# Performance work log

Measured on AMD Instinct MI355X. Metric: run time of the kernel, lower is better.

Reference implementation:

```python
import jax, jax.numpy as jnp
from jax import lax
import numpy as np

I, H, O = 4, 64, 4  # input_size, hidden_size, fc out


def setup_inputs() -> dict:
    key = jax.random.key(0)
    ks = jax.random.split(key, 7)
    B, T = 2048, 512
    s_ih = 1.0 / np.sqrt(H)  # PyTorch default init scale
    x = jax.random.normal(ks[0], (B, T, I), dtype=jnp.float32)
    W_ih = jax.random.uniform(ks[1], (4 * H, I), minval=-s_ih, maxval=s_ih, dtype=jnp.float32)
    W_hh = jax.random.uniform(ks[2], (4 * H, H), minval=-s_ih, maxval=s_ih, dtype=jnp.float32)
    b_ih = jax.random.uniform(ks[3], (4 * H,), minval=-s_ih, maxval=s_ih, dtype=jnp.float32)
    b_hh = jax.random.uniform(ks[4], (4 * H,), minval=-s_ih, maxval=s_ih, dtype=jnp.float32)
    W_fc = jax.random.uniform(ks[5], (O, H), minval=-s_ih, maxval=s_ih, dtype=jnp.float32)
    b_fc = jax.random.uniform(ks[6], (O,), minval=-s_ih, maxval=s_ih, dtype=jnp.float32)
    return {"x": x, "W_ih": W_ih, "W_hh": W_hh, "b_ih": b_ih, "b_hh": b_hh,
            "W_fc": W_fc, "b_fc": b_fc}


def reference(x, W_ih, W_hh, b_ih, b_hh, W_fc, b_fc):
    B = x.shape[0]
    # Precompute input contribution to all gates for every timestep: [B, T, 4H]
    xg = jnp.einsum('bti,gi->btg', x, W_ih) + (b_ih + b_hh)

    def step(carry, xt):
        h, c = carry                      # [B, H], [B, H]
        gates = xt + h @ W_hh.T           # [B, 4H]; PyTorch gate order i,f,g,o
        i, f, g, o = jnp.split(gates, 4, axis=-1)
        c = jax.nn.sigmoid(f) * c + jax.nn.sigmoid(i) * jnp.tanh(g)
        h = jax.nn.sigmoid(o) * jnp.tanh(c)
        return (h, c), None

    h0 = jnp.zeros((B, H), dtype=x.dtype)
    (h, c), _ = lax.scan(step, (h0, h0), jnp.swapaxes(xg, 0, 1))  # scan over T
    hidden = h[None]                      # [1, B, H] (num_layers*dirs = 1)
    return hidden @ W_fc.T + b_fc         # [1, B, O]
```

## Files before the change

kernel.cpp:

```cpp
#include <hip/hip_runtime.h>

typedef _Float16 half8 __attribute__((ext_vector_type(8)));
typedef _Float16 half4 __attribute__((ext_vector_type(4)));
typedef float f32x4 __attribute__((ext_vector_type(4)));

#define TT 512
#define HH 64
#define MB 4
#define S  88
#define XS 2056

__global__ __launch_bounds__(256, 2)
void lstm_v13(const float* __restrict__ x,
              const float* __restrict__ W_ih,
              const float* __restrict__ W_hh,
              const float* __restrict__ b_ih,
              const float* __restrict__ b_hh,
              const float* __restrict__ W_fc,
              const float* __restrict__ b_fc,
              float* __restrict__ out)
{
    __shared__ __align__(16) _Float16 st[2][MB * S];
    __shared__ __align__(16) _Float16 xbuf[MB * XS];

    const int tid = threadIdx.x;
    const int w   = tid >> 6;
    const int l   = tid & 63;
    const int q   = l >> 4;
    const int col = l & 15;
    const int bt  = col & 3;
    const int g   = col >> 2;
    const int b0  = blockIdx.x * MB;

    const float kN = -1.4426950408889634f;
    const float kP =  2.8853900817779268f;

    half8 aw[4][3];
    #pragma unroll
    for (int p = 0; p < 4; ++p) {
        const int r = 64 * (col & 3) + 16 * w + 4 * p + (col >> 2);
        const float scale = ((col & 3) == 2) ? kP : kN;
        #pragma unroll
        for (int c = 0; c < 2; ++c) {
            const float* src = W_hh + r * HH + 32 * c + 8 * q;
            half8 v;
            #pragma unroll
            for (int j = 0; j < 8; ++j) v[j] = (_Float16)(src[j] * scale);
            aw[p][c] = v;
        }
        half8 v = {};
        if (q == 0) {
            #pragma unroll
            for (int j = 0; j < 4; ++j) v[j] = (_Float16)(W_ih[r * 4 + j] * scale);
            v[4] = (_Float16)((b_ih[r] + b_hh[r]) * scale);
        }
        aw[p][2] = v;
    }

    #pragma unroll
    for (int it = 0; it < (MB * TT) / 256; ++it) {
        const int task = tid + it * 256;
        const int b = task >> 9, t = task & 511;
        float4 v = *(const float4*)(x + ((size_t)(b0 + b) * TT + t) * 4);
        half4 hx;
        hx[0] = (_Float16)v.x; hx[1] = (_Float16)v.y;
        hx[2] = (_Float16)v.z; hx[3] = (_Float16)v.w;
        *(half4*)&xbuf[b * XS + t * 4] = hx;
    }

    for (int i = tid; i < 2 * MB * S; i += 256) (&st[0][0])[i] = (_Float16)0.f;
    __syncthreads();

    float cs = 0.f;
    const int wrow = bt * S + 16 * w + 4 * g + q;
    const _Float16 hone = (_Float16)1.0f, hzer = (_Float16)0.f;
    const f32x4 z4 = {0.f, 0.f, 0.f, 0.f};
    const bool s1 = (g & 1) != 0, s2 = (g & 2) != 0;

    f32x4 accx0, accx1, accx2, accx3;
    {
        half4 xv = *(const half4*)&xbuf[bt * XS + 0];
        half8 bx = {xv[0], xv[1], xv[2], xv[3], hone, hzer, hzer, hzer};
        accx0 = __builtin_amdgcn_mfma_f32_16x16x32_f16(aw[0][2], bx, z4, 0, 0, 0);
        accx1 = __builtin_amdgcn_mfma_f32_16x16x32_f16(aw[1][2], bx, z4, 0, 0, 0);
        accx2 = __builtin_amdgcn_mfma_f32_16x16x32_f16(aw[2][2], bx, z4, 0, 0, 0);
        accx3 = __builtin_amdgcn_mfma_f32_16x16x32_f16(aw[3][2], bx, z4, 0, 0, 0);
    }

    #pragma unroll 4
    for (int t = 0; t < TT; ++t) {
        const int rb = t & 1, wb = rb ^ 1;
        const _Float16* sr = &st[rb][0];

        half8 bh0 = *(const half8*)&sr[bt * S +      8 * q];
        half8 bh1 = *(const half8*)&sr[bt * S + 32 + 8 * q];
        half4 xv2 = *(const half4*)&xbuf[bt * XS + (t + 1) * 4];

        f32x4 a0 = __builtin_amdgcn_mfma_f32_16x16x32_f16(aw[0][0], bh0, accx0, 0, 0, 0);
        f32x4 a1 = __builtin_amdgcn_mfma_f32_16x16x32_f16(aw[1][0], bh0, accx1, 0, 0, 0);
        f32x4 a2 = __builtin_amdgcn_mfma_f32_16x16x32_f16(aw[2][0], bh0, accx2, 0, 0, 0);
        f32x4 a3 = __builtin_amdgcn_mfma_f32_16x16x32_f16(aw[3][0], bh0, accx3, 0, 0, 0);
        a0 = __builtin_amdgcn_mfma_f32_16x16x32_f16(aw[0][1], bh1, a0, 0, 0, 0);
        a1 = __builtin_amdgcn_mfma_f32_16x16x32_f16(aw[1][1], bh1, a1, 0, 0, 0);
        a2 = __builtin_amdgcn_mfma_f32_16x16x32_f16(aw[2][1], bh1, a2, 0, 0, 0);
        a3 = __builtin_amdgcn_mfma_f32_16x16x32_f16(aw[3][1], bh1, a3, 0, 0, 0);

        {
            half8 bx2 = {xv2[0], xv2[1], xv2[2], xv2[3], hone, hzer, hzer, hzer};
            accx0 = __builtin_amdgcn_mfma_f32_16x16x32_f16(aw[0][2], bx2, z4, 0, 0, 0);
            accx1 = __builtin_amdgcn_mfma_f32_16x16x32_f16(aw[1][2], bx2, z4, 0, 0, 0);
            accx2 = __builtin_amdgcn_mfma_f32_16x16x32_f16(aw[2][2], bx2, z4, 0, 0, 0);
            accx3 = __builtin_amdgcn_mfma_f32_16x16x32_f16(aw[3][2], bx2, z4, 0, 0, 0);
        }

        #define SEL(j) (s2 ? (s1 ? a3[j] : a2[j]) : (s1 ? a1[j] : a0[j]))
        const float gi = SEL(0);
        const float gf = SEL(1);
        const float gg = SEL(2);
        const float go = SEL(3);
        #undef SEL

        const float EI = __builtin_amdgcn_exp2f(gi);
        const float EF = __builtin_amdgcn_exp2f(gf);
        const float EG = __builtin_amdgcn_exp2f(gg);
        const float rF = __builtin_amdgcn_rcpf(1.f + EF);
        const float r1 = __builtin_amdgcn_rcpf((1.f + EI) * (EG + 1.f));
        cs = cs * rF + (EG - 1.f) * r1;
        const float EO = __builtin_amdgcn_exp2f(go);
        const float EC = __builtin_amdgcn_exp2f(kP * cs);
        const float r2 = __builtin_amdgcn_rcpf((1.f + EO) * (EC + 1.f));
        const float hn = (EC - 1.f) * r2;

        st[wb][wrow] = (_Float16)hn;
        __syncthreads();
    }

    if (tid < MB * 4) {
        const int b = tid >> 2, o = tid & 3;
        float s = b_fc[o];
        const float* wf = W_fc + o * HH;
        #pragma unroll
        for (int k = 0; k < HH; ++k)
            s = fmaf((float)st[0][b * S + k], wf[k], s);
        out[(size_t)(b0 + b) * 4 + o] = s;
    }
}

extern "C" void kernel_launch(void* const* d_in, const int* in_sizes, int n_in,
                              void* d_out, int out_size, void* d_ws, size_t ws_size,
                              hipStream_t stream) {
    const float* x    = (const float*)d_in[0];
    const float* W_ih = (const float*)d_in[1];
    const float* W_hh = (const float*)d_in[2];
    const float* b_ih = (const float*)d_in[3];
    const float* b_hh = (const float*)d_in[4];
    const float* W_fc = (const float*)d_in[5];
    const float* b_fc = (const float*)d_in[6];
    float* out = (float*)d_out;
    lstm_v13<<<2048 / MB, 256, 0, stream>>>(x, W_ih, W_hh, b_ih, b_hh, W_fc, b_fc, out);
}
```

Before: 247.8 us.

## Split LSTM gate rows across 16 waves with 8 batches per block

Restructures the recurrent LSTM kernel to launch 1024-thread blocks holding 8 sequences each. Each wave now owns 4 hidden units (16 gate rows) and issues 3 MFMAs per step instead of 12. The MFMA columns carry 8 batches instead of 4 duplicated ones, which removes redundant matrix work and the per-lane gate-select logic. The cost is a block-wide barrier across 16 waves at every timestep, and half of the lanes compute duplicate columns that are never written.

```diff
diff --git a/kernel.cpp b/kernel.cpp
--- a/kernel.cpp
+++ b/kernel.cpp
@@ -6,12 +6,12 @@
 
 #define TT 512
 #define HH 64
-#define MB 4
-#define S  88
+#define MB 8
+#define S  80
 #define XS 2056
 
-__global__ __launch_bounds__(256, 2)
-void lstm_v13(const float* __restrict__ x,
+__global__ __launch_bounds__(1024, 1)
+void lstm_v14(const float* __restrict__ x,
               const float* __restrict__ W_ih,
               const float* __restrict__ W_hh,
               const float* __restrict__ b_ih,
@@ -28,17 +28,15 @@
     const int l   = tid & 63;
     const int q   = l >> 4;
     const int col = l & 15;
-    const int bt  = col & 3;
-    const int g   = col >> 2;
+    const int bt  = col & 7;
     const int b0  = blockIdx.x * MB;
 
     const float kN = -1.4426950408889634f;
     const float kP =  2.8853900817779268f;
 
-    half8 aw[4][3];
-    #pragma unroll
-    for (int p = 0; p < 4; ++p) {
-        const int r = 64 * (col & 3) + 16 * w + 4 * p + (col >> 2);
+    half8 aw[3];
+    {
+        const int r = 64 * (col & 3) + 4 * w + (col >> 2);
         const float scale = ((col & 3) == 2) ? kP : kN;
         #pragma unroll
         for (int c = 0; c < 2; ++c) {
@@ -46,7 +44,7 @@
             half8 v;
             #pragma unroll
             for (int j = 0; j < 8; ++j) v[j] = (_Float16)(src[j] * scale);
-            aw[p][c] = v;
+            aw[c] = v;
         }
         half8 v = {};
         if (q == 0) {
@@ -54,12 +52,12 @@
             for (int j = 0; j < 4; ++j) v[j] = (_Float16)(W_ih[r * 4 + j] * scale);
             v[4] = (_Float16)((b_ih[r] + b_hh[r]) * scale);
         }
-        aw[p][2] = v;
+        aw[2] = v;
     }
 
     #pragma unroll
-    for (int it = 0; it < (MB * TT) / 256; ++it) {
-        const int task = tid + it * 256;
+    for (int it = 0; it < (MB * TT) / 1024; ++it) {
+        const int task = tid + it * 1024;
         const int b = task >> 9, t = task & 511;
         float4 v = *(const float4*)(x + ((size_t)(b0 + b) * TT + t) * 4);
         half4 hx;
@@ -68,23 +66,20 @@
         *(half4*)&xbuf[b * XS + t * 4] = hx;
     }
 
-    for (int i = tid; i < 2 * MB * S; i += 256) (&st[0][0])[i] = (_Float16)0.f;
+    for (int i = tid; i < 2 * MB * S; i += 1024) (&st[0][0])[i] = (_Float16)0.f;
     __syncthreads();
 
     float cs = 0.f;
-    const int wrow = bt * S + 16 * w + 4 * g + q;
+    const int wrow = bt * S + 4 * w + q;
+    const bool writer = (col < 8);
     const _Float16 hone = (_Float16)1.0f, hzer = (_Float16)0.f;
     const f32x4 z4 = {0.f, 0.f, 0.f, 0.f};
-    const bool s1 = (g & 1) != 0, s2 = (g & 2) != 0;
 
-    f32x4 accx0, accx1, accx2, accx3;
+    f32x4 accx;
     {
         half4 xv = *(const half4*)&xbuf[bt * XS + 0];
         half8 bx = {xv[0], xv[1], xv[2], xv[3], hone, hzer, hzer, hzer};
-        accx0 = __builtin_amdgcn_mfma_f32_16x16x32_f16(aw[0][2], bx, z4, 0, 0, 0);
-        accx1 = __builtin_amdgcn_mfma_f32_16x16x32_f16(aw[1][2], bx, z4, 0, 0, 0);
-        accx2 = __builtin_amdgcn_mfma_f32_16x16x32_f16(aw[2][2], bx, z4, 0, 0, 0);
-        accx3 = __builtin_amdgcn_mfma_f32_16x16x32_f16(aw[3][2], bx, z4, 0, 0, 0);
+        accx = __builtin_amdgcn_mfma_f32_16x16x32_f16(aw[2], bx, z4, 0, 0, 0);
     }
 
     #pragma unroll 4
@@ -96,29 +91,18 @@
         half8 bh1 = *(const half8*)&sr[bt * S + 32 + 8 * q];
         half4 xv2 = *(const half4*)&xbuf[bt * XS + (t + 1) * 4];
 
-        f32x4 a0 = __builtin_amdgcn_mfma_f32_16x16x32_f16(aw[0][0], bh0, accx0, 0, 0, 0);
-        f32x4 a1 = __builtin_amdgcn_mfma_f32_16x16x32_f16(aw[1][0], bh0, accx1, 0, 0, 0);
-        f32x4 a2 = __builtin_amdgcn_mfma_f32_16x16x32_f16(aw[2][0], bh0, accx2, 0, 0, 0);
-        f32x4 a3 = __builtin_amdgcn_mfma_f32_16x16x32_f16(aw[3][0], bh0, accx3, 0, 0, 0);
-        a0 = __builtin_amdgcn_mfma_f32_16x16x32_f16(aw[0][1], bh1, a0, 0, 0, 0);
-        a1 = __builtin_amdgcn_mfma_f32_16x16x32_f16(aw[1][1], bh1, a1, 0, 0, 0);
-        a2 = __builtin_amdgcn_mfma_f32_16x16x32_f16(aw[2][1], bh1, a2, 0, 0, 0);
-        a3 = __builtin_amdgcn_mfma_f32_16x16x32_f16(aw[3][1], bh1, a3, 0, 0, 0);
+        f32x4 a0 = __builtin_amdgcn_mfma_f32_16x16x32_f16(aw[0], bh0, accx, 0, 0, 0);
+        a0 = __builtin_amdgcn_mfma_f32_16x16x32_f16(aw[1], bh1, a0, 0, 0, 0);
 
         {
             half8 bx2 = {xv2[0], xv2[1], xv2[2], xv2[3], hone, hzer, hzer, hzer};
-            accx0 = __builtin_amdgcn_mfma_f32_16x16x32_f16(aw[0][2], bx2, z4, 0, 0, 0);
-            accx1 = __builtin_amdgcn_mfma_f32_16x16x32_f16(aw[1][2], bx2, z4, 0, 0, 0);
-            accx2 = __builtin_amdgcn_mfma_f32_16x16x32_f16(aw[2][2], bx2, z4, 0, 0, 0);
-            accx3 = __builtin_amdgcn_mfma_f32_16x16x32_f16(aw[3][2], bx2, z4, 0, 0, 0);
+            accx = __builtin_amdgcn_mfma_f32_16x16x32_f16(aw[2], bx2, z4, 0, 0, 0);
         }
 
-        #define SEL(j) (s2 ? (s1 ? a3[j] : a2[j]) : (s1 ? a1[j] : a0[j]))
-        const float gi = SEL(0);
-        const float gf = SEL(1);
-        const float gg = SEL(2);
-        const float go = SEL(3);
-        #undef SEL
+        const float gi = a0[0];
+        const float gf = a0[1];
+        const float gg = a0[2];
+        const float go = a0[3];
 
         const float EI = __builtin_amdgcn_exp2f(gi);
         const float EF = __builtin_amdgcn_exp2f(gf);
@@ -131,7 +115,7 @@
         const float r2 = __builtin_amdgcn_rcpf((1.f + EO) * (EC + 1.f));
         const float hn = (EC - 1.f) * r2;
 
-        st[wb][wrow] = (_Float16)hn;
+        if (writer) st[wb][wrow] = (_Float16)hn;
         __syncthreads();
     }
 
@@ -157,5 +141,5 @@
     const float* W_fc = (const float*)d_in[5];
     const float* b_fc = (const float*)d_in[6];
     float* out = (float*)d_out;
-    lstm_v13<<<2048 / MB, 256, 0, stream>>>(x, W_ih, W_hh, b_ih, b_hh, W_fc, b_fc, out);
+    lstm_v14<<<2048 / MB, 1024, 0, stream>>>(x, W_ih, W_hh, b_ih, b_hh, W_fc, b_fc, out);
 }
```

New measurement: 247.7 us. Within noise of the previous version (-0.1%).

## Split LSTM hidden rows across eight waves with two MFMA tiles each

Applied to the files above, without the earlier changes.

The block grows from 4 to 8 wavefronts, and each wave now owns 8 hidden units, so it issues 2 gate tiles per step instead of 4. This shortens the serial per-step MFMA chain and cuts register use, which allows more blocks per CU. The x buffer is stored pre-padded as half8 with the bias one already in place, which removes per-step vector construction. In exchange, half the lanes compute redundant gate values that are never written, and the per-step barrier now synchronises twice as many waves.

```diff
diff --git a/kernel.cpp b/kernel.cpp
--- a/kernel.cpp
+++ b/kernel.cpp
@@ -7,11 +7,11 @@
 #define TT 512
 #define HH 64
 #define MB 4
-#define S  88
-#define XS 2056
+#define S  80
+#define XS 4104
 
-__global__ __launch_bounds__(256, 2)
-void lstm_v13(const float* __restrict__ x,
+__global__ __launch_bounds__(512, 4)
+void lstm_v15(const float* __restrict__ x,
               const float* __restrict__ W_ih,
               const float* __restrict__ W_hh,
               const float* __restrict__ b_ih,
@@ -29,16 +29,16 @@
     const int q   = l >> 4;
     const int col = l & 15;
     const int bt  = col & 3;
-    const int g   = col >> 2;
+    const int pbit = (col >> 2) & 1;
     const int b0  = blockIdx.x * MB;
 
     const float kN = -1.4426950408889634f;
     const float kP =  2.8853900817779268f;
 
-    half8 aw[4][3];
+    half8 aw[2][3];
     #pragma unroll
-    for (int p = 0; p < 4; ++p) {
-        const int r = 64 * (col & 3) + 16 * w + 4 * p + (col >> 2);
+    for (int p = 0; p < 2; ++p) {
+        const int r = 64 * (col & 3) + 8 * w + 2 * (col >> 2) + p;
         const float scale = ((col & 3) == 2) ? kP : kN;
         #pragma unroll
         for (int c = 0; c < 2; ++c) {
@@ -58,33 +58,31 @@
     }
 
     #pragma unroll
-    for (int it = 0; it < (MB * TT) / 256; ++it) {
-        const int task = tid + it * 256;
+    for (int it = 0; it < (MB * TT) / 512; ++it) {
+        const int task = tid + it * 512;
         const int b = task >> 9, t = task & 511;
         float4 v = *(const float4*)(x + ((size_t)(b0 + b) * TT + t) * 4);
-        half4 hx;
+        half8 hx;
         hx[0] = (_Float16)v.x; hx[1] = (_Float16)v.y;
         hx[2] = (_Float16)v.z; hx[3] = (_Float16)v.w;
-        *(half4*)&xbuf[b * XS + t * 4] = hx;
+        hx[4] = (_Float16)1.0f; hx[5] = (_Float16)0.f;
+        hx[6] = (_Float16)0.f;  hx[7] = (_Float16)0.f;
+        *(half8*)&xbuf[b * XS + t * 8] = hx;
     }
 
-    for (int i = tid; i < 2 * MB * S; i += 256) (&st[0][0])[i] = (_Float16)0.f;
+    for (int i = tid; i < 2 * MB * S; i += 512) (&st[0][0])[i] = (_Float16)0.f;
     __syncthreads();
 
     float cs = 0.f;
-    const int wrow = bt * S + 16 * w + 4 * g + q;
-    const _Float16 hone = (_Float16)1.0f, hzer = (_Float16)0.f;
+    const int wrow = bt * S + 8 * w + 2 * q + pbit;
+    const bool writer = (col < 8);
     const f32x4 z4 = {0.f, 0.f, 0.f, 0.f};
-    const bool s1 = (g & 1) != 0, s2 = (g & 2) != 0;
 
-    f32x4 accx0, accx1, accx2, accx3;
+    f32x4 accx0, accx1;
     {
-        half4 xv = *(const half4*)&xbuf[bt * XS + 0];
-        half8 bx = {xv[0], xv[1], xv[2], xv[3], hone, hzer, hzer, hzer};
+        half8 bx = *(const half8*)&xbuf[bt * XS + 0];
         accx0 = __builtin_amdgcn_mfma_f32_16x16x32_f16(aw[0][2], bx, z4, 0, 0, 0);
         accx1 = __builtin_amdgcn_mfma_f32_16x16x32_f16(aw[1][2], bx, z4, 0, 0, 0);
-        accx2 = __builtin_amdgcn_mfma_f32_16x16x32_f16(aw[2][2], bx, z4, 0, 0, 0);
-        accx3 = __builtin_amdgcn_mfma_f32_16x16x32_f16(aw[3][2], bx, z4, 0, 0, 0);
     }
 
     #pragma unroll 4
@@ -94,31 +92,20 @@
 
         half8 bh0 = *(const half8*)&sr[bt * S +      8 * q];
         half8 bh1 = *(const half8*)&sr[bt * S + 32 + 8 * q];
-        half4 xv2 = *(const half4*)&xbuf[bt * XS + (t + 1) * 4];
+        half8 bx2 = *(const half8*)&xbuf[bt * XS + (t + 1) * 8];
 
         f32x4 a0 = __builtin_amdgcn_mfma_f32_16x16x32_f16(aw[0][0], bh0, accx0, 0, 0, 0);
         f32x4 a1 = __builtin_amdgcn_mfma_f32_16x16x32_f16(aw[1][0], bh0, accx1, 0, 0, 0);
-        f32x4 a2 = __builtin_amdgcn_mfma_f32_16x16x32_f16(aw[2][0], bh0, accx2, 0, 0, 0);
-        f32x4 a3 = __builtin_amdgcn_mfma_f32_16x16x32_f16(aw[3][0], bh0, accx3, 0, 0, 0);
         a0 = __builtin_amdgcn_mfma_f32_16x16x32_f16(aw[0][1], bh1, a0, 0, 0, 0);
         a1 = __builtin_amdgcn_mfma_f32_16x16x32_f16(aw[1][1], bh1, a1, 0, 0, 0);
-        a2 = __builtin_amdgcn_mfma_f32_16x16x32_f16(aw[2][1], bh1, a2, 0, 0, 0);
-        a3 = __builtin_amdgcn_mfma_f32_16x16x32_f16(aw[3][1], bh1, a3, 0, 0, 0);
 
-        {
-            half8 bx2 = {xv2[0], xv2[1], xv2[2], xv2[3], hone, hzer, hzer, hzer};
-            accx0 = __builtin_amdgcn_mfma_f32_16x16x32_f16(aw[0][2], bx2, z4, 0, 0, 0);
-            accx1 = __builtin_amdgcn_mfma_f32_16x16x32_f16(aw[1][2], bx2, z4, 0, 0, 0);
-            accx2 = __builtin_amdgcn_mfma_f32_16x16x32_f16(aw[2][2], bx2, z4, 0, 0, 0);
-            accx3 = __builtin_amdgcn_mfma_f32_16x16x32_f16(aw[3][2], bx2, z4, 0, 0, 0);
-        }
+        accx0 = __builtin_amdgcn_mfma_f32_16x16x32_f16(aw[0][2], bx2, z4, 0, 0, 0);
+        accx1 = __builtin_amdgcn_mfma_f32_16x16x32_f16(aw[1][2], bx2, z4, 0, 0, 0);
 
-        #define SEL(j) (s2 ? (s1 ? a3[j] : a2[j]) : (s1 ? a1[j] : a0[j]))
-        const float gi = SEL(0);
-        const float gf = SEL(1);
-        const float gg = SEL(2);
-        const float go = SEL(3);
-        #undef SEL
+        const float gi = pbit ? a1[0] : a0[0];
+        const float gf = pbit ? a1[1] : a0[1];
+        const float gg = pbit ? a1[2] : a0[2];
+        const float go = pbit ? a1[3] : a0[3];
 
         const float EI = __builtin_amdgcn_exp2f(gi);
         const float EF = __builtin_amdgcn_exp2f(gf);
@@ -131,7 +118,7 @@
         const float r2 = __builtin_amdgcn_rcpf((1.f + EO) * (EC + 1.f));
         const float hn = (EC - 1.f) * r2;
 
-        st[wb][wrow] = (_Float16)hn;
+        if (writer) st[wb][wrow] = (_Float16)hn;
         __syncthreads();
     }
 
@@ -157,5 +144,5 @@
     const float* W_fc = (const float*)d_in[5];
     const float* b_fc = (const float*)d_in[6];
     float* out = (float*)d_out;
-    lstm_v13<<<2048 / MB, 256, 0, stream>>>(x, W_ih, W_hh, b_ih, b_hh, W_fc, b_fc, out);
+    lstm_v15<<<2048 / MB, 512, 0, stream>>>(x, W_ih, W_hh, b_ih, b_hh, W_fc, b_fc, out);
 }
```

New measurement: 279.6 us. 12.8% more time.
